# Kernel tuning notes

Hardware: AMD Instinct MI355X
Metric: run time of the kernel (lower is better)

The kernel has to match this reference:

```python
import jax, jax.numpy as jnp
import numpy as np

B, Q, K = 4, 1024, 1024
QS, KS, H, V = 512, 512, 32, 256


def setup_inputs() -> dict:
    key = jax.random.key(0)
    ks = jax.random.split(key, 6)
    return {
        "queries": jax.random.normal(ks[0], (B, Q, QS), dtype=jnp.float32),
        "keys": jax.random.normal(ks[1], (B, K, KS), dtype=jnp.float32),
        "values": jax.random.normal(ks[2], (B, K, V), dtype=jnp.float32),
        "Wq": jax.random.normal(ks[3], (QS, H), dtype=jnp.float32) / np.sqrt(QS),
        "Wk": jax.random.normal(ks[4], (KS, H), dtype=jnp.float32) / np.sqrt(KS),
        "wv": jax.random.normal(ks[5], (H,), dtype=jnp.float32) / np.sqrt(H),
    }


def reference(queries, keys, values, Wq, Wk, wv):
    # projections
    q = jnp.einsum("bqe,eh->bqh", queries, Wq)  # [B,Q,H]
    k = jnp.einsum("bke,eh->bkh", keys, Wk)     # [B,K,H]
    # additive (Bahdanau) scoring: broadcast add -> tanh -> linear score
    feats = jnp.tanh(q[:, :, None, :] + k[:, None, :, :])  # [B,Q,K,H]
    scores = jnp.einsum("bqkh,h->bqk", feats, wv)           # [B,Q,K]
    attn = jax.nn.softmax(scores, axis=-1)                   # softmax over keys
    # dropout p=0.0 (eval) -> identity
    return jnp.einsum("bqk,bkv->bqv", attn, values)          # [B,Q,V]
```

## Files before the change

### kernel.cpp

```cpp
#include <hip/hip_runtime.h>

#define BATCH 4
#define QDIM 1024
#define KDIM 1024
#define EDIM 512
#define H 32
#define VDIM 256
#define QT 16

#define TWO_LOG2E 2.8853900817779268f
#define LOG2E 1.4426950408889634f

typedef __attribute__((ext_vector_type(8))) short short8;
typedef __attribute__((ext_vector_type(4))) float f32x4;
typedef __attribute__((ext_vector_type(2))) float f32x2;

typedef __attribute__((address_space(3))) void lds_void_t;
typedef __attribute__((address_space(1))) const void gbl_cvoid_t;

static __device__ __forceinline__ void gll16(const void* g, void* l) {
    __builtin_amdgcn_global_load_lds((gbl_cvoid_t*)g, (lds_void_t*)l, 16, 0, 0);
}

static __device__ __forceinline__ unsigned short f32_to_bf16(float f) {
    unsigned int bits = __float_as_uint(f);
    return (unsigned short)((bits + 0x7FFFu + ((bits >> 16) & 1u)) >> 16);
}

static __device__ __forceinline__ unsigned int pack_bf16(float a, float b) {
    unsigned int ua = __float_as_uint(a) + 0x8000u;
    unsigned int ub = __float_as_uint(b) + 0x8000u;
    return __builtin_amdgcn_perm(ub, ua, 0x07060302u);
}

__global__ __launch_bounds__(256) void prep_kernel(
    const float* __restrict__ qin, const float* __restrict__ kin,
    const float* __restrict__ Wqm, const float* __restrict__ Wkm,
    const float* __restrict__ values,
    float* __restrict__ qp, float* __restrict__ kp,
    unsigned short* __restrict__ vt)
{
    __shared__ float t[64][65];
    __shared__ f32x4 lacc[2][64][2];
    __shared__ unsigned short wlds[32][520];
    const int tid = (int)threadIdx.x;
    const int bid = (int)blockIdx.x;

    if (bid < 256) {
        const int wave = tid >> 6, lane = tid & 63;
        const int tile = wave >> 1;
        const int khalf = wave & 1;
        const int grow = bid * 32 + tile * 16;
        const bool is_k = grow >= 4096;
        const float* X = is_k ? kin : qin;
        const float* W = is_k ? Wkm : Wqm;
        const int row0 = is_k ? grow - 4096 : grow;
        const int arow = lane & 15, aq = lane >> 4;

        for (int i = 0; i < 64; ++i) {
            const int idx = i * 256 + tid;
            wlds[idx & 31][idx >> 5] = f32_to_bf16(W[idx]);
        }
        __syncthreads();

        const float* xrow = X + (size_t)(row0 + arow) * EDIM + khalf * 256 + aq * 8;
        const unsigned short* wt0 = &wlds[arow][khalf * 256 + aq * 8];
        const unsigned short* wt1 = &wlds[arow + 16][khalf * 256 + aq * 8];

        f32x4 acc0 = {0.f, 0.f, 0.f, 0.f};
        f32x4 acc1 = {0.f, 0.f, 0.f, 0.f};
        #pragma unroll
        for (int s = 0; s < 8; ++s) {
            float4 xa = *reinterpret_cast<const float4*>(xrow + s * 32);
            float4 xb = *reinterpret_cast<const float4*>(xrow + s * 32 + 4);
            unsigned int p0 = pack_bf16(xa.x, xa.y);
            unsigned int p1 = pack_bf16(xa.z, xa.w);
            unsigned int p2 = pack_bf16(xb.x, xb.y);
            unsigned int p3 = pack_bf16(xb.z, xb.w);
            uint4 au = make_uint4(p0, p1, p2, p3);
            short8 af = *reinterpret_cast<const short8*>(&au);
            short8 b0 = *reinterpret_cast<const short8*>(wt0 + s * 32);
            short8 b1 = *reinterpret_cast<const short8*>(wt1 + s * 32);
            acc0 = __builtin_amdgcn_mfma_f32_16x16x32_bf16(af, b0, acc0, 0, 0, 0);
            acc1 = __builtin_amdgcn_mfma_f32_16x16x32_bf16(af, b1, acc1, 0, 0, 0);
        }
        if (khalf == 1) {
            lacc[tile][lane][0] = acc0;
            lacc[tile][lane][1] = acc1;
        }
        __syncthreads();
        if (khalf == 0) {
            f32x4 o0 = lacc[tile][lane][0];
            f32x4 o1 = lacc[tile][lane][1];
            acc0 += o0; acc1 += o1;
            if (is_k) {
                #pragma unroll
                for (int r = 0; r < 4; ++r) {
                    const int row = aq * 4 + r;
                    float* orow = kp + (size_t)(row0 + row) * H;
                    orow[arow]      = __builtin_amdgcn_exp2f(acc0[r] * TWO_LOG2E);
                    orow[arow + 16] = __builtin_amdgcn_exp2f(acc1[r] * TWO_LOG2E);
                }
            } else {
                float* tbase = qp + (size_t)(row0 >> 4) * 512;
                #pragma unroll
                for (int r = 0; r < 4; ++r) {
                    const int row = aq * 4 + r;
                    tbase[arow * 16 + row]        = __builtin_amdgcn_exp2f(acc0[r] * TWO_LOG2E);
                    tbase[(arow + 16) * 16 + row] = __builtin_amdgcn_exp2f(acc1[r] * TWO_LOG2E);
                }
            }
        }
    } else {
        const int pid  = bid - 256;
        const int xcd  = pid & 7, slot = pid >> 3;
        const int b    = xcd >> 1;
        const int tnum = slot * 2 + (xcd & 1);
        const int kt = tnum & 15, ct = tnum >> 4;
        const int k0 = kt * 64, c0 = ct * 64;
        const int col4 = (tid & 15) * 4;
        const int krow = tid >> 4;

        #pragma unroll
        for (int i = 0; i < 4; ++i) {
            const int kk = i * 16 + krow;
            float4 v = *reinterpret_cast<const float4*>(
                values + ((size_t)(b * KDIM + k0 + kk) * VDIM + c0 + col4));
            t[kk][col4 + 0] = v.x; t[kk][col4 + 1] = v.y;
            t[kk][col4 + 2] = v.z; t[kk][col4 + 3] = v.w;
        }
        __syncthreads();

        const int col = tid >> 2;
        const int ks  = (tid & 3) * 16;
        unsigned int pk[8];
        #pragma unroll
        for (int j = 0; j < 8; ++j) {
            unsigned int lo = f32_to_bf16(t[ks + 2 * j][col]);
            unsigned int hi = f32_to_bf16(t[ks + 2 * j + 1][col]);
            pk[j] = lo | (hi << 16);
        }
        const int colg = c0 + col;
        const int w_ = colg >> 4, arow_ = colg & 15;
        const int kA = k0 + ks, kB = kA + 8;
        uint4* vt4 = reinterpret_cast<uint4*>(vt);
        const size_t idxA = ((size_t)(b * 16 + w_) * 32 + (kA >> 5)) * 64
                            + ((kA >> 3) & 3) * 16 + arow_;
        const size_t idxB = ((size_t)(b * 16 + w_) * 32 + (kB >> 5)) * 64
                            + ((kB >> 3) & 3) * 16 + arow_;
        vt4[idxA] = make_uint4(pk[0], pk[1], pk[2], pk[3]);
        vt4[idxB] = make_uint4(pk[4], pk[5], pk[6], pk[7]);
    }
}

__global__ __launch_bounds__(1024, 4) void attn_fused(
    const float* __restrict__ qp, const float* __restrict__ kp,
    const unsigned short* __restrict__ vt, const float* __restrict__ wv,
    float* __restrict__ out)
{
    __shared__ __align__(16) unsigned char a_lds[32 * 1024];
    __shared__ __align__(16) unsigned char slab[16 * 4 * 1024];
    __shared__ float inv_lds[QT];

    const int tid = (int)threadIdx.x;
    const int pid = (int)blockIdx.x;
    const int xcd = pid & 7, slot = pid >> 3;
    const int b   = xcd >> 1;
    const int tnum = slot * 2 + (xcd & 1);
    const int q0  = tnum * QT;

    float sumwv = 0.f;
    #pragma unroll
    for (int h = 0; h < H; ++h) sumwv += wv[h];
    const float c0s = sumwv * LOG2E;
    const float c1s = 2.0f * LOG2E;

    {
        const int kk   = tid;
        const int base = (kk >> 5) * 1024 + (kk & 31) * 2;
        float kreg[H];
        const float* krow = kp + (size_t)(b * KDIM + kk) * H;
        #pragma unroll
        for (int i = 0; i < H / 4; ++i) {
            float4 v = *reinterpret_cast<const float4*>(krow + i * 4);
            kreg[i * 4 + 0] = v.x; kreg[i * 4 + 1] = v.y;
            kreg[i * 4 + 2] = v.z; kreg[i * 4 + 3] = v.w;
        }
        const float* eqt = qp + (size_t)((b << 6) | tnum) * 512;

        for (int p = 0; p < 8; ++p) {
            f32x2 s2e = {0.f, 0.f}, s2o = {0.f, 0.f};
            #pragma unroll
            for (int g = 0; g < 8; ++g) {
                const int h = g * 4;
                f32x2 e0 = *reinterpret_cast<const f32x2*>(eqt + (h + 0) * 16 + 2 * p);
                f32x2 e1 = *reinterpret_cast<const f32x2*>(eqt + (h + 1) * 16 + 2 * p);
                f32x2 e2 = *reinterpret_cast<const f32x2*>(eqt + (h + 2) * 16 + 2 * p);
                f32x2 e3 = *reinterpret_cast<const f32x2*>(eqt + (h + 3) * 16 + 2 * p);
                const f32x2 one = {1.f, 1.f};
                f32x2 U0 = e0 * (f32x2){kreg[h + 0], kreg[h + 0]} + one;
                f32x2 U1 = e1 * (f32x2){kreg[h + 1], kreg[h + 1]} + one;
                f32x2 U2 = e2 * (f32x2){kreg[h + 2], kreg[h + 2]} + one;
                f32x2 U3 = e3 * (f32x2){kreg[h + 3], kreg[h + 3]} + one;
                f32x2 n01 = U1 * (f32x2){wv[h + 0], wv[h + 0]}
                          + U0 * (f32x2){wv[h + 1], wv[h + 1]};
                f32x2 n23 = U3 * (f32x2){wv[h + 2], wv[h + 2]}
                          + U2 * (f32x2){wv[h + 3], wv[h + 3]};
                f32x2 d01 = U0 * U1;
                f32x2 d23 = U2 * U3;
                f32x2 n = n01 * d23 + n23 * d01;
                f32x2 d = d01 * d23;
                f32x2 r;
                r.x = __builtin_amdgcn_rcpf(d.x);
                r.y = __builtin_amdgcn_rcpf(d.y);
                if (g & 1) s2o += n * r; else s2e += n * r;
            }
            f32x2 s2 = s2e + s2o;
            float wgtA = __builtin_amdgcn_exp2f(fmaf(-c1s, s2.x, c0s));
            float wgtB = __builtin_amdgcn_exp2f(fmaf(-c1s, s2.y, c0s));
            const int qrA = 2 * p, qrB = 2 * p + 1;
            const int addrA = (base + qrA * 64) ^ ((qrA & 7) << 4);
            const int addrB = (base + qrB * 64) ^ ((qrB & 7) << 4);
            *reinterpret_cast<unsigned short*>(a_lds + addrA) = f32_to_bf16(wgtA);
            *reinterpret_cast<unsigned short*>(a_lds + addrB) = f32_to_bf16(wgtB);
        }
    }
    __syncthreads();

    {
        const int row = tid >> 6;
        const int c   = tid & 63;
        float s = 0.f;
        #pragma unroll
        for (int j = 0; j < 16; ++j) {
            const int k = c + j * 64;
            const int addr = ((k >> 5) * 1024 + row * 64 + (k & 31) * 2)
                             ^ ((row & 7) << 4);
            unsigned int u = *reinterpret_cast<const unsigned short*>(a_lds + addr);
            s += __uint_as_float(u << 16);
        }
        #pragma unroll
        for (int m = 32; m > 0; m >>= 1) s += __shfl_xor(s, m, 64);
        if (c == 0) inv_lds[row] = 1.0f / s;
    }
    __syncthreads();

    const int w    = tid >> 6;
    const int lane = tid & 63;
    const int colb = w * 16;
    const int arow = lane & 15;
    const int aq   = lane >> 4;
    f32x4 acc = {0.f, 0.f, 0.f, 0.f};
    {
        const char* gsrc = reinterpret_cast<const char*>(vt)
                         + ((size_t)(b * 16 + w) * 32) * 1024 + lane * 16;
        char* lbase = reinterpret_cast<char*>(slab) + w * 4096;

        #pragma unroll
        for (int d = 0; d < 3; ++d)
            gll16(gsrc + d * 1024, lbase + d * 1024);

        #pragma unroll 4
        for (int kc = 0; kc < 29; ++kc) {
            gll16(gsrc + (kc + 3) * 1024, lbase + ((kc + 3) & 3) * 1024);
            asm volatile("s_waitcnt vmcnt(3)" ::: "memory");
            const int aaddr = (kc * 1024 + arow * 64 + aq * 16) ^ ((arow & 7) << 4);
            short8 af = *reinterpret_cast<const short8*>(a_lds + aaddr);
            short8 bv = *reinterpret_cast<const short8*>(lbase + (kc & 3) * 1024 + lane * 16);
            acc = __builtin_amdgcn_mfma_f32_16x16x32_bf16(af, bv, acc, 0, 0, 0);
        }
        #define PV_TAIL(KC, VC) { \
            asm volatile("s_waitcnt vmcnt(" #VC ")" ::: "memory"); \
            const int aaddr = ((KC) * 1024 + arow * 64 + aq * 16) ^ ((arow & 7) << 4); \
            short8 af = *reinterpret_cast<const short8*>(a_lds + aaddr); \
            short8 bv = *reinterpret_cast<const short8*>(lbase + ((KC) & 3) * 1024 + lane * 16); \
            acc = __builtin_amdgcn_mfma_f32_16x16x32_bf16(af, bv, acc, 0, 0, 0); }
        PV_TAIL(29, 2)
        PV_TAIL(30, 1)
        PV_TAIL(31, 0)
        #undef PV_TAIL
    }

    __syncthreads();
    {
        float* otile = reinterpret_cast<float*>(a_lds);
        #pragma unroll
        for (int r = 0; r < 4; ++r) {
            const int row = aq * 4 + r;
            otile[row * 264 + colb + arow] = acc[r] * inv_lds[row];
        }
    }
    __syncthreads();
    {
        const float* otile = reinterpret_cast<const float*>(a_lds);
        const int row = tid >> 6;
        const int c4  = (tid & 63) * 4;
        f32x4 v = *reinterpret_cast<const f32x4*>(&otile[row * 264 + c4]);
        *reinterpret_cast<f32x4*>(out + (size_t)(b * QDIM + q0 + row) * VDIM + c4) = v;
    }
}

extern "C" void kernel_launch(void* const* d_in, const int* in_sizes, int n_in,
                              void* d_out, int out_size, void* d_ws, size_t ws_size,
                              hipStream_t stream) {
    const float* queries = (const float*)d_in[0];
    const float* keys    = (const float*)d_in[1];
    const float* values  = (const float*)d_in[2];
    const float* Wq      = (const float*)d_in[3];
    const float* Wk      = (const float*)d_in[4];
    const float* wv      = (const float*)d_in[5];
    float* out = (float*)d_out;

    float* qp = (float*)d_ws;
    float* kp = qp + (size_t)BATCH * QDIM * H;
    unsigned short* vt = (unsigned short*)(kp + (size_t)BATCH * KDIM * H);

    hipLaunchKernelGGL(prep_kernel, dim3(512), dim3(256), 0, stream,
                       queries, keys, Wq, Wk, values, qp, kp, vt);
    hipLaunchKernelGGL(attn_fused, dim3(BATCH * (QDIM / QT)), dim3(1024), 0, stream,
                       qp, kp, vt, wv, out);
}
```

Baseline: 31.81 us.

## Precompute bf16 transposed weights once and split projection K across four waves

Adds a small kernel that converts Wq/Wk to bf16 and transposes them into workspace once, instead of every projection block converting the full weight matrix into LDS. The projection blocks now each handle 16 rows with the 512-wide reduction split across four waves, reduced through LDS, which doubles the projection block count. Weights are read directly from global/L2 rather than LDS. The cost is an extra kernel launch and a serial dependency before the prep kernel.

```diff
diff --git a/kernel.cpp b/kernel.cpp
--- a/kernel.cpp
+++ b/kernel.cpp
@@ -33,44 +33,47 @@
     return __builtin_amdgcn_perm(ub, ua, 0x07060302u);
 }
 
+__global__ __launch_bounds__(256) void wprep_kernel(
+    const float* __restrict__ Wqm, const float* __restrict__ Wkm,
+    unsigned short* __restrict__ wtq, unsigned short* __restrict__ wtk)
+{
+    const bool is_k = blockIdx.x >= 64;
+    const float* W = is_k ? Wkm : Wqm;
+    unsigned short* Wt = is_k ? wtk : wtq;
+    const int idx = ((int)blockIdx.x & 63) * 256 + (int)threadIdx.x;
+    const int e = idx >> 5, c = idx & 31;
+    Wt[(size_t)c * EDIM + e] = f32_to_bf16(W[idx]);
+}
+
 __global__ __launch_bounds__(256) void prep_kernel(
     const float* __restrict__ qin, const float* __restrict__ kin,
-    const float* __restrict__ Wqm, const float* __restrict__ Wkm,
+    const unsigned short* __restrict__ wtq, const unsigned short* __restrict__ wtk,
     const float* __restrict__ values,
     float* __restrict__ qp, float* __restrict__ kp,
     unsigned short* __restrict__ vt)
 {
     __shared__ float t[64][65];
-    __shared__ f32x4 lacc[2][64][2];
-    __shared__ unsigned short wlds[32][520];
+    __shared__ f32x4 lacc[3][64][2];
     const int tid = (int)threadIdx.x;
     const int bid = (int)blockIdx.x;
 
-    if (bid < 256) {
+    if (bid < 512) {
         const int wave = tid >> 6, lane = tid & 63;
-        const int tile = wave >> 1;
-        const int khalf = wave & 1;
-        const int grow = bid * 32 + tile * 16;
-        const bool is_k = grow >= 4096;
+        const bool is_k = bid >= 256;
         const float* X = is_k ? kin : qin;
-        const float* W = is_k ? Wkm : Wqm;
-        const int row0 = is_k ? grow - 4096 : grow;
+        const unsigned short* Wt = is_k ? wtk : wtq;
+        const int row0 = (bid & 255) * 16;
         const int arow = lane & 15, aq = lane >> 4;
-
-        for (int i = 0; i < 64; ++i) {
-            const int idx = i * 256 + tid;
-            wlds[idx & 31][idx >> 5] = f32_to_bf16(W[idx]);
-        }
-        __syncthreads();
-
-        const float* xrow = X + (size_t)(row0 + arow) * EDIM + khalf * 256 + aq * 8;
-        const unsigned short* wt0 = &wlds[arow][khalf * 256 + aq * 8];
-        const unsigned short* wt1 = &wlds[arow + 16][khalf * 256 + aq * 8];
+        const int koff = wave * 128 + aq * 8;
+
+        const float* xrow = X + (size_t)(row0 + arow) * EDIM + koff;
+        const unsigned short* wt0 = Wt + (size_t)arow * EDIM + koff;
+        const unsigned short* wt1 = Wt + (size_t)(arow + 16) * EDIM + koff;
 
         f32x4 acc0 = {0.f, 0.f, 0.f, 0.f};
         f32x4 acc1 = {0.f, 0.f, 0.f, 0.f};
         #pragma unroll
-        for (int s = 0; s < 8; ++s) {
+        for (int s = 0; s < 4; ++s) {
             float4 xa = *reinterpret_cast<const float4*>(xrow + s * 32);
             float4 xb = *reinterpret_cast<const float4*>(xrow + s * 32 + 4);
             unsigned int p0 = pack_bf16(xa.x, xa.y);
@@ -84,15 +87,17 @@
             acc0 = __builtin_amdgcn_mfma_f32_16x16x32_bf16(af, b0, acc0, 0, 0, 0);
             acc1 = __builtin_amdgcn_mfma_f32_16x16x32_bf16(af, b1, acc1, 0, 0, 0);
         }
-        if (khalf == 1) {
-            lacc[tile][lane][0] = acc0;
-            lacc[tile][lane][1] = acc1;
+        if (wave != 0) {
+            lacc[wave - 1][lane][0] = acc0;
+            lacc[wave - 1][lane][1] = acc1;
         }
         __syncthreads();
-        if (khalf == 0) {
-            f32x4 o0 = lacc[tile][lane][0];
-            f32x4 o1 = lacc[tile][lane][1];
-            acc0 += o0; acc1 += o1;
+        if (wave == 0) {
+            #pragma unroll
+            for (int j = 0; j < 3; ++j) {
+                acc0 += lacc[j][lane][0];
+                acc1 += lacc[j][lane][1];
+            }
             if (is_k) {
                 #pragma unroll
                 for (int r = 0; r < 4; ++r) {
@@ -112,7 +117,7 @@
             }
         }
     } else {
-        const int pid  = bid - 256;
+        const int pid  = bid - 512;
         const int xcd  = pid & 7, slot = pid >> 3;
         const int b    = xcd >> 1;
         const int tnum = slot * 2 + (xcd & 1);
@@ -313,10 +318,13 @@
 
     float* qp = (float*)d_ws;
     float* kp = qp + (size_t)BATCH * QDIM * H;
-    unsigned short* vt = (unsigned short*)(kp + (size_t)BATCH * KDIM * H);
-
-    hipLaunchKernelGGL(prep_kernel, dim3(512), dim3(256), 0, stream,
-                       queries, keys, Wq, Wk, values, qp, kp, vt);
+    unsigned short* vt  = (unsigned short*)(kp + (size_t)BATCH * KDIM * H);
+    unsigned short* wtq = vt + (size_t)BATCH * VDIM * KDIM;
+    unsigned short* wtk = wtq + (size_t)H * EDIM;
+
+    hipLaunchKernelGGL(wprep_kernel, dim3(128), dim3(256), 0, stream, Wq, Wk, wtq, wtk);
+    hipLaunchKernelGGL(prep_kernel, dim3(768), dim3(256), 0, stream,
+                       queries, keys, wtq, wtk, values, qp, kp, vt);
     hipLaunchKernelGGL(attn_fused, dim3(BATCH * (QDIM / QT)), dim3(1024), 0, stream,
                        qp, kp, vt, wv, out);
 }
```

Measured after the change: 36.78 us. 1.16x slower.
